# Kernel optimization log

Measured on AMD Instinct MI355X. Metric: run time of the kernel, lower is better.

The kernel has to match this reference:

```python
import jax, jax.numpy as jnp
import numpy as np

N_NODES = 100000
N_EDGES = 1600000
IN_DIM = 128
HID_DIM = 32
OUT_DIM = 64
N_REL = 8
N_CLASSES = 2


def setup_inputs() -> dict:
    key = jax.random.key(0)
    ks = jax.random.split(key, 12)
    x = jax.random.normal(ks[0], (N_NODES, IN_DIM), dtype=jnp.float32)
    edge_index = jax.random.randint(ks[1], (2, N_EDGES), 0, N_NODES, dtype=jnp.int64)
    edge_type = jax.random.randint(ks[2], (N_EDGES,), 0, N_REL, dtype=jnp.int64)
    # FastRGCNConv params: per-relation weight W [R, in, out], root weight, bias
    def glorot(k, shape):
        fan_in, fan_out = shape[-2], shape[-1]
        s = jnp.sqrt(6.0 / (fan_in + fan_out))
        return jax.random.uniform(k, shape, jnp.float32, -s, s)
    W1 = glorot(ks[3], (N_REL, IN_DIM, HID_DIM))
    root1 = glorot(ks[4], (IN_DIM, HID_DIM))
    b1 = jnp.zeros((HID_DIM,), jnp.float32)
    W2 = glorot(ks[5], (N_REL, HID_DIM, OUT_DIM))
    root2 = glorot(ks[6], (HID_DIM, OUT_DIM))
    b2 = jnp.zeros((OUT_DIM,), jnp.float32)
    lin_w = glorot(ks[7], (OUT_DIM, N_CLASSES))
    lin_b = jnp.zeros((N_CLASSES,), jnp.float32)
    return {"x": x, "edge_index": edge_index, "edge_type": edge_type,
            "W1": W1, "root1": root1, "b1": b1,
            "W2": W2, "root2": root2, "b2": b2,
            "lin_w": lin_w, "lin_b": lin_b}


def _fast_rgcn_conv(x, W, root, b, src, dst, etype, n_nodes):
    """FastRGCNConv: per-relation transform, gather by (src, relation),
    mean-aggregate by destination, plus root transform and bias."""
    # Transform all nodes by all relation weights: [N, R, H]
    xW = jnp.einsum('nf,rfh->nrh', x, W)
    # Per-edge message: relation-specific transformed source feature [E, H]
    msg = xW[src, etype]
    agg = jax.ops.segment_sum(msg, dst, num_segments=n_nodes)
    deg = jax.ops.segment_sum(jnp.ones((src.shape[0],), x.dtype), dst,
                              num_segments=n_nodes)
    agg = agg / jnp.maximum(deg, 1.0)[:, None]  # mean aggregation
    return agg + x @ root + b


def reference(x, edge_index, edge_type, W1, root1, b1, W2, root2, b2, lin_w, lin_b):
    src, dst = edge_index[0], edge_index[1]
    n = x.shape[0]
    h = jax.nn.relu(_fast_rgcn_conv(x, W1, root1, b1, src, dst, edge_type, n))
    h = _fast_rgcn_conv(h, W2, root2, b2, src, dst, edge_type, n)
    return h @ lin_w + lin_b
```

## Files before the change

kernel.cpp:

```cpp
#include <hip/hip_runtime.h>

#define NN      100000
#define IN_DIM  128
#define HID     32
#define ODIM    64
#define L1C     288
#define L2K     288
#define NWGS    196
#define NCB     784
#define CCAP    40
#define RECCAP  2304
#define G2ST    296
#define PST     40
#define HST     40

using bf16x8 = __attribute__((ext_vector_type(8))) short;
using f32x4  = __attribute__((ext_vector_type(4))) float;

__device__ __forceinline__ float bf2f(short s) {
    unsigned int u = ((unsigned int)(unsigned short)s) << 16;
    float f; __builtin_memcpy(&f, &u, 4); return f;
}
__device__ __forceinline__ short f2bf(float f) {
    unsigned int u; __builtin_memcpy(&u, &f, 4);
    u += 0x7fffu + ((u >> 16) & 1u);
    return (short)(u >> 16);
}
__device__ __forceinline__ float ldf(const void* p, int i, int f32) {
    return f32 ? ((const float*)p)[i] : bf2f(((const short*)p)[i]);
}
__device__ __forceinline__ int ldi(const int* p, long long i, int i64) {
    return i64 ? p[2 * i] : p[(int)i];
}

__global__ __launch_bounds__(1024) void detect(const short* __restrict__ x,
                                               const short* __restrict__ W1,
                                               const short* __restrict__ r1,
                                               const short* __restrict__ W2,
                                               const short* __restrict__ r2,
                                               const short* __restrict__ lw,
                                               const int* __restrict__ ei,
                                               const int* __restrict__ et,
                                               int* __restrict__ flags) {
    __shared__ int cnt[8];
    if (threadIdx.x < 8) cnt[threadIdx.x] = 0;
    __syncthreads();
    const short* ptrs[6] = {x, W1, r1, W2, r2, lw};
    const int    nsmp[6] = {1024, 1024, 1024, 1024, 1024, 64};
    int t = threadIdx.x;
#pragma unroll
    for (int j = 0; j < 6; ++j) {
        if (t < nsmp[j]) {
            unsigned int s = (unsigned short)ptrs[j][2 * t];
            unsigned int e = (s >> 7) & 0xFF;
            if (e >= 140u || (e >= 1u && e <= 100u)) atomicAdd(&cnt[j], 1);
        }
    }
    if (t < 128) {
        if (ei[2 * t + 1] != 0) atomicAdd(&cnt[6], 1);
        if (et[2 * t + 1] != 0) atomicAdd(&cnt[7], 1);
    }
    __syncthreads();
    if (t == 0) {
        const int ns[6] = {1024, 1024, 1024, 1024, 1024, 64};
        for (int j = 0; j < 6; ++j) flags[j] = (cnt[j] * 4 > ns[j]) ? 1 : 0;
        flags[6] = (cnt[6] == 0) ? 1 : 0;
        flags[7] = (cnt[7] == 0) ? 1 : 0;
    }
}

__global__ __launch_bounds__(256) void prep_w1(const void* __restrict__ W1,
                                               const void* __restrict__ root1,
                                               short* __restrict__ w1t,
                                               const int* __restrict__ flags) {
    int i = blockIdx.x * 256 + threadIdx.x;
    if (i >= L1C * IN_DIM) return;
    int c = i >> 7, f = i & 127;
    float v;
    if (c < 256) { int r = c >> 5, h = c & 31; v = ldf(W1, (r * IN_DIM + f) * HID + h, flags[1]); }
    else         { v = ldf(root1, f * HID + (c - 256), flags[2]); }
    w1t[c * IN_DIM + f] = f2bf(v);
}
__global__ __launch_bounds__(256) void prep_w2c(const void* __restrict__ W2,
                                                const void* __restrict__ root2,
                                                short* __restrict__ w2ct,
                                                const int* __restrict__ flags) {
    int i = blockIdx.x * 256 + threadIdx.x;
    if (i >= ODIM * L2K) return;
    int c = i / L2K, k = i % L2K;
    float v;
    if (k < 256) { int r = k >> 5, kk = k & 31; v = ldf(W2, (r * HID + kk) * ODIM + c, flags[3]); }
    else         { v = ldf(root2, (k - 256) * ODIM + c, flags[4]); }
    w2ct[c * L2K + k] = f2bf(v);
}
__global__ __launch_bounds__(256) void prep_small(const short* __restrict__ b1,
                                                  const short* __restrict__ b2,
                                                  const void* __restrict__ lin_w,
                                                  const short* __restrict__ lin_b,
                                                  short* __restrict__ smallc,
                                                  const int* __restrict__ flags) {
    int i = threadIdx.x;
    if (i < 32)        smallc[i] = b1[i];
    else if (i < 96)   smallc[i] = b2[i - 32];
    else if (i < 224)  smallc[i] = f2bf(ldf(lin_w, i - 96, flags[5]));
    else if (i < 226)  smallc[i] = lin_b[i - 224];
}

__global__ __launch_bounds__(1024) void scatter_coarse(const int* __restrict__ ei,
                                                       const int* __restrict__ et,
                                                       int* __restrict__ cnt,
                                                       int* __restrict__ seg, int E,
                                                       const int* __restrict__ flags) {
    __shared__ int cur[NCB];
    if (threadIdx.x < NCB) cur[threadIdx.x] = 0;
    __syncthreads();
    int i64 = flags[6], t64 = flags[7];
    int epw = (E + NWGS - 1) / NWGS;
    int lo = blockIdx.x * epw;
    int hi = lo + epw; if (hi > E) hi = E;
    for (int i = lo + threadIdx.x; i < hi; i += 1024) {
        int s = ldi(ei, i, i64);
        int d = ldi(ei, (long long)E + i, i64);
        int r = ldi(et, i, t64);
        int cb = d >> 7;
        int pos = atomicAdd(&cur[cb], 1);
        if (pos < CCAP)
            seg[(cb * NWGS + (int)blockIdx.x) * CCAP + pos] = ((d & 127) << 20) | (s << 3) | r;
    }
    __syncthreads();
    if (threadIdx.x < NCB) {
        int c = cur[threadIdx.x];
        cnt[blockIdx.x * NCB + threadIdx.x] = c < CCAP ? c : CCAP;
    }
}

__global__ __launch_bounds__(64) void cb_sum(const int* __restrict__ cnt,
                                             int* __restrict__ cbTot) {
    int cb = blockIdx.x, lane = threadIdx.x;
    int t = 0;
    for (int g = lane; g < NWGS; g += 64) t += cnt[g * NCB + cb];
#pragma unroll
    for (int o = 32; o > 0; o >>= 1) t += __shfl_down(t, o, 64);
    if (lane == 0) cbTot[cb] = t;
}

__global__ __launch_bounds__(1024) void cb_scan2(const int* __restrict__ cbTot,
                                                 int* __restrict__ cbBase,
                                                 int* __restrict__ off) {
    __shared__ int s[1024];
    int t = threadIdx.x;
    int v = (t < NCB) ? cbTot[t] : 0;
    s[t] = v; __syncthreads();
    for (int o = 1; o < 1024; o <<= 1) {
        int u = (t >= o) ? s[t - o] : 0;
        __syncthreads();
        s[t] += u;
        __syncthreads();
    }
    if (t < NCB) cbBase[t] = s[t] - v;
    if (t == NCB - 1) off[NN] = s[t];
}

__global__ __launch_bounds__(256) void build_cb(const int* __restrict__ cnt,
                                                const int* __restrict__ seg,
                                                const int* __restrict__ cbBase,
                                                int* __restrict__ off,
                                                float* __restrict__ inv_deg,
                                                int* __restrict__ packed) {
    __shared__ int cntl[NWGS], soff[NWGS];
    __shared__ int recs[RECCAP];
    __shared__ int degl[128], basel[128], kcur[128];
    __shared__ int stmp[256];
    int cb = blockIdx.x, tid = threadIdx.x;
    if (tid < NWGS) cntl[tid] = cnt[tid * NCB + cb];
    if (tid < 128) degl[tid] = 0;
    __syncthreads();
    int v = (tid < NWGS) ? cntl[tid] : 0;
    stmp[tid] = v; __syncthreads();
    for (int o = 1; o < 256; o <<= 1) {
        int u = (tid >= o) ? stmp[tid - o] : 0;
        __syncthreads();
        stmp[tid] += u;
        __syncthreads();
    }
    if (tid < NWGS) soff[tid] = stmp[tid] - v;
    int tot = stmp[255]; if (tot > RECCAP) tot = RECCAP;
    __syncthreads();
    int wave = tid >> 6, lane = tid & 63;
    for (int g = wave; g < NWGS; g += 4) {
        int c = cntl[g], b = soff[g];
        const int* sp = seg + (cb * NWGS + g) * CCAP;
        for (int e = lane; e < c; e += 64)
            if (b + e < RECCAP) recs[b + e] = sp[e];
    }
    __syncthreads();
    for (int i = tid; i < tot; i += 256) atomicAdd(&degl[recs[i] >> 20], 1);
    __syncthreads();
    int dv = (tid < 128) ? degl[tid] : 0;
    stmp[tid] = dv; __syncthreads();
    for (int o = 1; o < 128; o <<= 1) {
        int u = (tid >= o) ? stmp[tid - o] : 0;
        __syncthreads();
        stmp[tid] += u;
        __syncthreads();
    }
    int gbase = cbBase[cb];
    if (tid < 128) {
        int excl = stmp[tid] - dv;
        basel[tid] = excl;
        kcur[tid] = 0;
        int node = cb * 128 + tid;
        if (node < NN) {
            off[node] = gbase + excl;
            inv_deg[node] = 1.0f / (float)(dv > 1 ? dv : 1);
        }
    }
    __syncthreads();
    for (int i = tid; i < tot; i += 256) {
        int rec = recs[i];
        int n = rec >> 20;
        int p = atomicAdd(&kcur[n], 1);
        packed[gbase + basel[n] + p] = ((n & 15) << 24) | (rec & 0xFFFFF);
    }
}

__global__ __launch_bounds__(256) void gemm1(const void* __restrict__ x,
                                             const short* __restrict__ w1t,
                                             short* __restrict__ xw,
                                             const int* __restrict__ flags) {
    int wave = threadIdx.x >> 6, lane = threadIdx.x & 63;
    int m = lane & 15, quad = lane >> 4;
    int row0 = (blockIdx.x * 4 + wave) * 64;
    if (row0 >= NN) return;

    bf16x8 a[4][4];
    int fp32 = flags[0];
#pragma unroll
    for (int t = 0; t < 4; ++t) {
        int row = row0 + t * 16 + m;
        int rc = row < NN ? row : NN - 1;
        if (fp32) {
            const float* xr = (const float*)x + rc * IN_DIM + quad * 8;
#pragma unroll
            for (int kt = 0; kt < 4; ++kt) {
                const f32x4* q = (const f32x4*)(xr + kt * 32);
                f32x4 u0 = q[0], u1 = q[1];
                bf16x8 tt;
                tt[0] = f2bf(u0[0]); tt[1] = f2bf(u0[1]); tt[2] = f2bf(u0[2]); tt[3] = f2bf(u0[3]);
                tt[4] = f2bf(u1[0]); tt[5] = f2bf(u1[1]); tt[6] = f2bf(u1[2]); tt[7] = f2bf(u1[3]);
                a[t][kt] = tt;
            }
        } else {
            const short* xr = (const short*)x + rc * IN_DIM + quad * 8;
#pragma unroll
            for (int kt = 0; kt < 4; ++kt) a[t][kt] = *(const bf16x8*)(xr + kt * 32);
        }
    }

    for (int ct = 0; ct < 18; ++ct) {
        const short* wp = w1t + (ct * 16 + m) * IN_DIM + quad * 8;
        bf16x8 b[4];
#pragma unroll
        for (int kt = 0; kt < 4; ++kt) b[kt] = *(const bf16x8*)(wp + kt * 32);
#pragma unroll
        for (int t = 0; t < 4; ++t) {
            f32x4 acc = {0.f, 0.f, 0.f, 0.f};
#pragma unroll
            for (int kt = 0; kt < 4; ++kt)
                acc = __builtin_amdgcn_mfma_f32_16x16x32_bf16(a[t][kt], b[kt], acc, 0, 0, 0);
#pragma unroll
            for (int i = 0; i < 4; ++i) {
                int r = row0 + t * 16 + quad * 4 + i;
                if (r < NN) xw[r * L1C + ct * 16 + m] = f2bf(acc[i]);
            }
        }
    }
}

__global__ __launch_bounds__(256) void agg1(const short* __restrict__ xw,
                                            const int* __restrict__ off,
                                            const int* __restrict__ packed,
                                            const float* __restrict__ inv_deg,
                                            const short* __restrict__ smallc,
                                            short* __restrict__ h) {
    int lane = threadIdx.x & 31;
    int node = blockIdx.x * 8 + (threadIdx.x >> 5);
    if (node >= NN) return;
    int s = off[node], e = off[node + 1];
    float acc = 0.f;
    int i = s;
    for (; i + 3 < e; i += 4) {
        int pk0 = packed[i], pk1 = packed[i + 1], pk2 = packed[i + 2], pk3 = packed[i + 3];
        float v0 = bf2f(xw[((pk0 >> 3) & 0x1FFFF) * L1C + (pk0 & 7) * 32 + lane]);
        float v1 = bf2f(xw[((pk1 >> 3) & 0x1FFFF) * L1C + (pk1 & 7) * 32 + lane]);
        float v2 = bf2f(xw[((pk2 >> 3) & 0x1FFFF) * L1C + (pk2 & 7) * 32 + lane]);
        float v3 = bf2f(xw[((pk3 >> 3) & 0x1FFFF) * L1C + (pk3 & 7) * 32 + lane]);
        acc += (v0 + v1) + (v2 + v3);
    }
    for (; i < e; ++i) {
        int pk = packed[i];
        acc += bf2f(xw[((pk >> 3) & 0x1FFFF) * L1C + (pk & 7) * 32 + lane]);
    }
    float v = acc * inv_deg[node] + bf2f(xw[node * L1C + 256 + lane]) + bf2f(smallc[lane]);
    h[node * HID + lane] = f2bf(v > 0.f ? v : 0.f);
}

__global__ __launch_bounds__(256) void agg2_fused(const short* __restrict__ h,
                                                  const int* __restrict__ off,
                                                  const int* __restrict__ packed,
                                                  const float* __restrict__ inv_deg,
                                                  const short* __restrict__ w2ct,
                                                  const short* __restrict__ smallc,
                                                  float* __restrict__ out) {
    __shared__ __align__(16) short Pl[128 * PST];
    __shared__ __align__(16) short HgT[32 * HST];
    __shared__ __align__(16) short g2l[16 * G2ST];
    __shared__ float red[4][16][2];
    __shared__ float invl[16];
    int tid = threadIdx.x;
    int row0 = blockIdx.x * 16;
    if (tid < 16) invl[tid] = inv_deg[row0 + tid];
    int st = off[row0], en = off[row0 + 16];

    int wave = tid >> 6, lane = tid & 63;
    int m15 = lane & 15, quad = lane >> 4;
    int e = tid & 31;
    int part = tid >> 5;

    {
        uint4 z = {0, 0, 0, 0};
        uint4* pz = (uint4*)Pl;
#pragma unroll
        for (int j = 0; j < 2; ++j) pz[tid + j * 256] = z;
        if (tid < 128) pz[tid + 512] = z;
    }

    f32x4 acc00 = {0,0,0,0}, acc01 = {0,0,0,0}, acc10 = {0,0,0,0}, acc11 = {0,0,0,0};
    int prevrow = -1;

    for (int c0 = st; c0 < en; c0 += 32) {
        int idx = c0 + e;
        int pk = (idx < en) ? packed[idx] : 0;
        int src = (pk >> 3) & 0x1FFFF;
        uint2 hv = *(const uint2*)(h + src * HID + part * 4);
        __syncthreads();
        if (tid < 32 && prevrow >= 0) Pl[prevrow * PST + e] = 0;
        short hs0 = (short)(hv.x & 0xFFFF), hs1 = (short)(hv.x >> 16);
        short hs2 = (short)(hv.y & 0xFFFF), hs3 = (short)(hv.y >> 16);
        HgT[(part * 4 + 0) * HST + e] = hs0;
        HgT[(part * 4 + 1) * HST + e] = hs1;
        HgT[(part * 4 + 2) * HST + e] = hs2;
        HgT[(part * 4 + 3) * HST + e] = hs3;
        if (tid < 32) {
            if (idx < en) {
                int row = ((pk >> 24) & 15) * 8 + (pk & 7);
                Pl[row * PST + e] = (short)0x3F80;
                prevrow = row;
            } else prevrow = -1;
        }
        __syncthreads();
        bf16x8 a0 = *(const bf16x8*)(&HgT[m15 * HST + quad * 8]);
        bf16x8 a1 = *(const bf16x8*)(&HgT[(m15 + 16) * HST + quad * 8]);
        bf16x8 b0 = *(const bf16x8*)(&Pl[((wave * 2 + 0) * 16 + m15) * PST + quad * 8]);
        bf16x8 b1 = *(const bf16x8*)(&Pl[((wave * 2 + 1) * 16 + m15) * PST + quad * 8]);
        acc00 = __builtin_amdgcn_mfma_f32_16x16x32_bf16(a0, b0, acc00, 0, 0, 0);
        acc10 = __builtin_amdgcn_mfma_f32_16x16x32_bf16(a1, b0, acc10, 0, 0, 0);
        acc01 = __builtin_amdgcn_mfma_f32_16x16x32_bf16(a0, b1, acc01, 0, 0, 0);
        acc11 = __builtin_amdgcn_mfma_f32_16x16x32_bf16(a1, b1, acc11, 0, 0, 0);
    }
    __syncthreads();

    {
        int nr0 = (wave * 2 + 0) * 16 + m15;
        int nr1 = (wave * 2 + 1) * 16 + m15;
        float sc0 = invl[nr0 >> 3], sc1 = invl[nr1 >> 3];
        int d0 = quad * 4;
#pragma unroll
        for (int i = 0; i < 4; ++i) {
            g2l[(nr0 >> 3) * G2ST + (nr0 & 7) * 32 + d0 + i]      = f2bf(acc00[i] * sc0);
            g2l[(nr0 >> 3) * G2ST + (nr0 & 7) * 32 + 16 + d0 + i] = f2bf(acc10[i] * sc0);
            g2l[(nr1 >> 3) * G2ST + (nr1 & 7) * 32 + d0 + i]      = f2bf(acc01[i] * sc1);
            g2l[(nr1 >> 3) * G2ST + (nr1 & 7) * 32 + 16 + d0 + i] = f2bf(acc11[i] * sc1);
        }
    }
    for (int j = tid; j < 16 * 32; j += 256) {
        int node = j >> 5, d = j & 31;
        g2l[node * G2ST + 256 + d] = h[(row0 + node) * HID + d];
    }
    __syncthreads();

    const short* wp = w2ct + (wave * 16 + m15) * L2K + quad * 8;
    bf16x8 a[9], b[9];
#pragma unroll
    for (int kt = 0; kt < 9; ++kt) {
        b[kt] = *(const bf16x8*)(wp + kt * 32);
        a[kt] = *(const bf16x8*)(&g2l[m15 * G2ST + quad * 8 + kt * 32]);
    }
    f32x4 acc = {0.f, 0.f, 0.f, 0.f};
#pragma unroll
    for (int kt = 0; kt < 9; ++kt)
        acc = __builtin_amdgcn_mfma_f32_16x16x32_bf16(a[kt], b[kt], acc, 0, 0, 0);

    int c = wave * 16 + m15;
    float lw0 = bf2f(smallc[96 + c * 2 + 0]);
    float lw1 = bf2f(smallc[96 + c * 2 + 1]);
    float b2c = bf2f(smallc[32 + c]);
    float pr0[4], pr1[4];
#pragma unroll
    for (int i = 0; i < 4; ++i) {
        float v = acc[i] + b2c;
        pr0[i] = v * lw0;
        pr1[i] = v * lw1;
    }
#pragma unroll
    for (int o = 1; o < 16; o <<= 1) {
#pragma unroll
        for (int i = 0; i < 4; ++i) {
            pr0[i] += __shfl_xor(pr0[i], o, 64);
            pr1[i] += __shfl_xor(pr1[i], o, 64);
        }
    }
    if (m15 == 0) {
#pragma unroll
        for (int i = 0; i < 4; ++i) {
            red[wave][quad * 4 + i][0] = pr0[i];
            red[wave][quad * 4 + i][1] = pr1[i];
        }
    }
    __syncthreads();
    if (tid < 32) {
        int row = tid >> 1, j = tid & 1;
        float v = red[0][row][j] + red[1][row][j] + red[2][row][j] + red[3][row][j]
                + bf2f(smallc[224 + j]);
        out[(row0 + row) * 2 + j] = v;
    }
}

extern "C" void kernel_launch(void* const* d_in, const int* in_sizes, int n_in,
                              void* d_out, int out_size, void* d_ws, size_t ws_size,
                              hipStream_t stream) {
    const void* x     = d_in[0];
    const int*  ei    = (const int*)d_in[1];
    const int*  etype = (const int*)d_in[2];
    const void* W1    = d_in[3];
    const void* root1 = d_in[4];
    const void* b1    = d_in[5];
    const void* W2    = d_in[6];
    const void* root2 = d_in[7];
    const void* b2    = d_in[8];
    const void* lin_w = d_in[9];
    const void* lin_b = d_in[10];
    float* out = (float*)d_out;

    const int E = in_sizes[2];

    char* p = (char*)d_ws;
    auto alloc = [&](size_t bytes) { char* r = p; p += (bytes + 255) & ~(size_t)255; return (void*)r; };
    int*   flags   = (int*)  alloc(256);
    int*   off     = (int*)  alloc((size_t)(NN + 1) * 4);
    float* inv_deg = (float*)alloc((size_t)NN * 4);
    int*   packed  = (int*)  alloc((size_t)E * 4);
    int*   cnt     = (int*)  alloc((size_t)NWGS * NCB * 4);
    int*   cbTot   = (int*)  alloc((size_t)NCB * 4);
    int*   cbBase  = (int*)  alloc((size_t)NCB * 4);
    int*   seg     = (int*)  alloc((size_t)NCB * NWGS * CCAP * 4);
    short* w1t     = (short*)alloc((size_t)L1C * IN_DIM * 2);
    short* w2ct    = (short*)alloc((size_t)ODIM * L2K * 2);
    short* smallc  = (short*)alloc(256 * 2);
    short* h       = (short*)alloc((size_t)NN * HID * 2);
    short* xw1     = (short*)alloc((size_t)NN * L1C * 2);

    detect<<<1, 1024, 0, stream>>>((const short*)x, (const short*)W1, (const short*)root1,
                                   (const short*)W2, (const short*)root2, (const short*)lin_w,
                                   ei, etype, flags);
    prep_w1<<<(L1C * IN_DIM + 255) / 256, 256, 0, stream>>>(W1, root1, w1t, flags);
    prep_w2c<<<(ODIM * L2K + 255) / 256, 256, 0, stream>>>(W2, root2, w2ct, flags);
    prep_small<<<1, 256, 0, stream>>>((const short*)b1, (const short*)b2, lin_w,
                                      (const short*)lin_b, smallc, flags);

    scatter_coarse<<<NWGS, 1024, 0, stream>>>(ei, etype, cnt, seg, E, flags);
    cb_sum<<<NCB, 64, 0, stream>>>(cnt, cbTot);
    cb_scan2<<<1, 1024, 0, stream>>>(cbTot, cbBase, off);
    build_cb<<<NCB, 256, 0, stream>>>(cnt, seg, cbBase, off, inv_deg, packed);

    gemm1<<<((NN + 63) / 64 + 3) / 4, 256, 0, stream>>>(x, w1t, xw1, flags);
    agg1<<<(NN + 7) / 8, 256, 0, stream>>>(xw1, off, packed, inv_deg, smallc, h);
    agg2_fused<<<NN / 16, 256, 0, stream>>>(h, off, packed, inv_deg, w2ct, smallc, out);
}
```

Measured before the change: 310.1 us.

## Merge weight-prep kernels and co-launch gemm1 with edge scatter; unroll agg1 by 8

Folds the three weight-preparation kernels into one launch. It also moves the independent edge coarse-scatter into the same grid as the first GEMM, using extra blocks, so the two overlap on the GPU and fewer kernels are launched. The scatter blocks drop from 1024 to 256 threads, so each scatter block processes its edge slice more slowly. agg1 gains an 8-way unrolled gather loop to keep more loads in flight.

```diff
diff --git a/kernel.cpp b/kernel.cpp
--- a/kernel.cpp
+++ b/kernel.cpp
@@ -69,68 +69,124 @@
     }
 }
 
-__global__ __launch_bounds__(256) void prep_w1(const void* __restrict__ W1,
-                                               const void* __restrict__ root1,
-                                               short* __restrict__ w1t,
-                                               const int* __restrict__ flags) {
-    int i = blockIdx.x * 256 + threadIdx.x;
-    if (i >= L1C * IN_DIM) return;
-    int c = i >> 7, f = i & 127;
-    float v;
-    if (c < 256) { int r = c >> 5, h = c & 31; v = ldf(W1, (r * IN_DIM + f) * HID + h, flags[1]); }
-    else         { v = ldf(root1, f * HID + (c - 256), flags[2]); }
-    w1t[c * IN_DIM + f] = f2bf(v);
-}
-__global__ __launch_bounds__(256) void prep_w2c(const void* __restrict__ W2,
+__global__ __launch_bounds__(256) void prep_all(const void* __restrict__ W1,
+                                                const void* __restrict__ root1,
+                                                const void* __restrict__ W2,
                                                 const void* __restrict__ root2,
+                                                const short* __restrict__ b1,
+                                                const short* __restrict__ b2,
+                                                const void* __restrict__ lin_w,
+                                                const short* __restrict__ lin_b,
+                                                short* __restrict__ w1t,
                                                 short* __restrict__ w2ct,
+                                                short* __restrict__ smallc,
                                                 const int* __restrict__ flags) {
-    int i = blockIdx.x * 256 + threadIdx.x;
-    if (i >= ODIM * L2K) return;
-    int c = i / L2K, k = i % L2K;
-    float v;
-    if (k < 256) { int r = k >> 5, kk = k & 31; v = ldf(W2, (r * HID + kk) * ODIM + c, flags[3]); }
-    else         { v = ldf(root2, (k - 256) * ODIM + c, flags[4]); }
-    w2ct[c * L2K + k] = f2bf(v);
-}
-__global__ __launch_bounds__(256) void prep_small(const short* __restrict__ b1,
-                                                  const short* __restrict__ b2,
-                                                  const void* __restrict__ lin_w,
-                                                  const short* __restrict__ lin_b,
-                                                  short* __restrict__ smallc,
-                                                  const int* __restrict__ flags) {
-    int i = threadIdx.x;
-    if (i < 32)        smallc[i] = b1[i];
-    else if (i < 96)   smallc[i] = b2[i - 32];
-    else if (i < 224)  smallc[i] = f2bf(ldf(lin_w, i - 96, flags[5]));
-    else if (i < 226)  smallc[i] = lin_b[i - 224];
-}
-
-__global__ __launch_bounds__(1024) void scatter_coarse(const int* __restrict__ ei,
-                                                       const int* __restrict__ et,
-                                                       int* __restrict__ cnt,
-                                                       int* __restrict__ seg, int E,
-                                                       const int* __restrict__ flags) {
-    __shared__ int cur[NCB];
-    if (threadIdx.x < NCB) cur[threadIdx.x] = 0;
-    __syncthreads();
-    int i64 = flags[6], t64 = flags[7];
-    int epw = (E + NWGS - 1) / NWGS;
-    int lo = blockIdx.x * epw;
-    int hi = lo + epw; if (hi > E) hi = E;
-    for (int i = lo + threadIdx.x; i < hi; i += 1024) {
-        int s = ldi(ei, i, i64);
-        int d = ldi(ei, (long long)E + i, i64);
-        int r = ldi(et, i, t64);
-        int cb = d >> 7;
-        int pos = atomicAdd(&cur[cb], 1);
-        if (pos < CCAP)
-            seg[(cb * NWGS + (int)blockIdx.x) * CCAP + pos] = ((d & 127) << 20) | (s << 3) | r;
-    }
-    __syncthreads();
-    if (threadIdx.x < NCB) {
-        int c = cur[threadIdx.x];
-        cnt[blockIdx.x * NCB + threadIdx.x] = c < CCAP ? c : CCAP;
+    int gi = blockIdx.x * 256 + threadIdx.x;
+    if (gi < L1C * IN_DIM) {
+        int c = gi >> 7, f = gi & 127;
+        float v;
+        if (c < 256) { int r = c >> 5, h = c & 31; v = ldf(W1, (r * IN_DIM + f) * HID + h, flags[1]); }
+        else         { v = ldf(root1, f * HID + (c - 256), flags[2]); }
+        w1t[c * IN_DIM + f] = f2bf(v);
+        return;
+    }
+    int i2 = gi - L1C * IN_DIM;
+    if (i2 < ODIM * L2K) {
+        int c = i2 / L2K, k = i2 % L2K;
+        float v;
+        if (k < 256) { int r = k >> 5, kk = k & 31; v = ldf(W2, (r * HID + kk) * ODIM + c, flags[3]); }
+        else         { v = ldf(root2, (k - 256) * ODIM + c, flags[4]); }
+        w2ct[c * L2K + k] = f2bf(v);
+        return;
+    }
+    int i3 = i2 - ODIM * L2K;
+    if (i3 < 256) {
+        if (i3 < 32)        smallc[i3] = b1[i3];
+        else if (i3 < 96)   smallc[i3] = b2[i3 - 32];
+        else if (i3 < 224)  smallc[i3] = f2bf(ldf(lin_w, i3 - 96, flags[5]));
+        else if (i3 < 226)  smallc[i3] = lin_b[i3 - 224];
+    }
+}
+
+__global__ __launch_bounds__(256) void gemm1_scatter(const void* __restrict__ x,
+                                                     const short* __restrict__ w1t,
+                                                     short* __restrict__ xw,
+                                                     const int* __restrict__ ei,
+                                                     const int* __restrict__ et,
+                                                     int* __restrict__ cnt,
+                                                     int* __restrict__ seg, int E,
+                                                     const int* __restrict__ flags, int G1) {
+    if ((int)blockIdx.x >= G1) {
+        __shared__ int cur[NCB];
+        for (int k = threadIdx.x; k < NCB; k += 256) cur[k] = 0;
+        __syncthreads();
+        int bid = blockIdx.x - G1;
+        int i64 = flags[6], t64 = flags[7];
+        int epw = (E + NWGS - 1) / NWGS;
+        int lo = bid * epw;
+        int hi = lo + epw; if (hi > E) hi = E;
+        for (int i = lo + threadIdx.x; i < hi; i += 256) {
+            int s = ldi(ei, i, i64);
+            int d = ldi(ei, (long long)E + i, i64);
+            int r = ldi(et, i, t64);
+            int cb = d >> 7;
+            int pos = atomicAdd(&cur[cb], 1);
+            if (pos < CCAP)
+                seg[(cb * NWGS + bid) * CCAP + pos] = ((d & 127) << 20) | (s << 3) | r;
+        }
+        __syncthreads();
+        for (int k = threadIdx.x; k < NCB; k += 256) {
+            int c = cur[k];
+            cnt[bid * NCB + k] = c < CCAP ? c : CCAP;
+        }
+        return;
+    }
+    int wave = threadIdx.x >> 6, lane = threadIdx.x & 63;
+    int m = lane & 15, quad = lane >> 4;
+    int row0 = (blockIdx.x * 4 + wave) * 64;
+    if (row0 >= NN) return;
+
+    bf16x8 a[4][4];
+    int fp32 = flags[0];
+#pragma unroll
+    for (int t = 0; t < 4; ++t) {
+        int row = row0 + t * 16 + m;
+        int rc = row < NN ? row : NN - 1;
+        if (fp32) {
+            const float* xr = (const float*)x + rc * IN_DIM + quad * 8;
+#pragma unroll
+            for (int kt = 0; kt < 4; ++kt) {
+                const f32x4* q = (const f32x4*)(xr + kt * 32);
+                f32x4 u0 = q[0], u1 = q[1];
+                bf16x8 tt;
+                tt[0] = f2bf(u0[0]); tt[1] = f2bf(u0[1]); tt[2] = f2bf(u0[2]); tt[3] = f2bf(u0[3]);
+                tt[4] = f2bf(u1[0]); tt[5] = f2bf(u1[1]); tt[6] = f2bf(u1[2]); tt[7] = f2bf(u1[3]);
+                a[t][kt] = tt;
+            }
+        } else {
+            const short* xr = (const short*)x + rc * IN_DIM + quad * 8;
+#pragma unroll
+            for (int kt = 0; kt < 4; ++kt) a[t][kt] = *(const bf16x8*)(xr + kt * 32);
+        }
+    }
+
+    for (int ct = 0; ct < 18; ++ct) {
+        const short* wp = w1t + (ct * 16 + m) * IN_DIM + quad * 8;
+        bf16x8 b[4];
+#pragma unroll
+        for (int kt = 0; kt < 4; ++kt) b[kt] = *(const bf16x8*)(wp + kt * 32);
+#pragma unroll
+        for (int t = 0; t < 4; ++t) {
+            f32x4 acc = {0.f, 0.f, 0.f, 0.f};
+#pragma unroll
+            for (int kt = 0; kt < 4; ++kt)
+                acc = __builtin_amdgcn_mfma_f32_16x16x32_bf16(a[t][kt], b[kt], acc, 0, 0, 0);
+#pragma unroll
+            for (int i = 0; i < 4; ++i) {
+                int r = row0 + t * 16 + quad * 4 + i;
+                if (r < NN) xw[r * L1C + ct * 16 + m] = f2bf(acc[i]);
+            }
+        }
     }
 }
 
@@ -224,59 +280,6 @@
     }
 }
 
-__global__ __launch_bounds__(256) void gemm1(const void* __restrict__ x,
-                                             const short* __restrict__ w1t,
-                                             short* __restrict__ xw,
-                                             const int* __restrict__ flags) {
-    int wave = threadIdx.x >> 6, lane = threadIdx.x & 63;
-    int m = lane & 15, quad = lane >> 4;
-    int row0 = (blockIdx.x * 4 + wave) * 64;
-    if (row0 >= NN) return;
-
-    bf16x8 a[4][4];
-    int fp32 = flags[0];
-#pragma unroll
-    for (int t = 0; t < 4; ++t) {
-        int row = row0 + t * 16 + m;
-        int rc = row < NN ? row : NN - 1;
-        if (fp32) {
-            const float* xr = (const float*)x + rc * IN_DIM + quad * 8;
-#pragma unroll
-            for (int kt = 0; kt < 4; ++kt) {
-                const f32x4* q = (const f32x4*)(xr + kt * 32);
-                f32x4 u0 = q[0], u1 = q[1];
-                bf16x8 tt;
-                tt[0] = f2bf(u0[0]); tt[1] = f2bf(u0[1]); tt[2] = f2bf(u0[2]); tt[3] = f2bf(u0[3]);
-                tt[4] = f2bf(u1[0]); tt[5] = f2bf(u1[1]); tt[6] = f2bf(u1[2]); tt[7] = f2bf(u1[3]);
-                a[t][kt] = tt;
-            }
-        } else {
-            const short* xr = (const short*)x + rc * IN_DIM + quad * 8;
-#pragma unroll
-            for (int kt = 0; kt < 4; ++kt) a[t][kt] = *(const bf16x8*)(xr + kt * 32);
-        }
-    }
-
-    for (int ct = 0; ct < 18; ++ct) {
-        const short* wp = w1t + (ct * 16 + m) * IN_DIM + quad * 8;
-        bf16x8 b[4];
-#pragma unroll
-        for (int kt = 0; kt < 4; ++kt) b[kt] = *(const bf16x8*)(wp + kt * 32);
-#pragma unroll
-        for (int t = 0; t < 4; ++t) {
-            f32x4 acc = {0.f, 0.f, 0.f, 0.f};
-#pragma unroll
-            for (int kt = 0; kt < 4; ++kt)
-                acc = __builtin_amdgcn_mfma_f32_16x16x32_bf16(a[t][kt], b[kt], acc, 0, 0, 0);
-#pragma unroll
-            for (int i = 0; i < 4; ++i) {
-                int r = row0 + t * 16 + quad * 4 + i;
-                if (r < NN) xw[r * L1C + ct * 16 + m] = f2bf(acc[i]);
-            }
-        }
-    }
-}
-
 __global__ __launch_bounds__(256) void agg1(const short* __restrict__ xw,
                                             const int* __restrict__ off,
                                             const int* __restrict__ packed,
@@ -289,6 +292,19 @@
     int s = off[node], e = off[node + 1];
     float acc = 0.f;
     int i = s;
+    for (; i + 7 < e; i += 8) {
+        int pk0 = packed[i],     pk1 = packed[i + 1], pk2 = packed[i + 2], pk3 = packed[i + 3];
+        int pk4 = packed[i + 4], pk5 = packed[i + 5], pk6 = packed[i + 6], pk7 = packed[i + 7];
+        float v0 = bf2f(xw[((pk0 >> 3) & 0x1FFFF) * L1C + (pk0 & 7) * 32 + lane]);
+        float v1 = bf2f(xw[((pk1 >> 3) & 0x1FFFF) * L1C + (pk1 & 7) * 32 + lane]);
+        float v2 = bf2f(xw[((pk2 >> 3) & 0x1FFFF) * L1C + (pk2 & 7) * 32 + lane]);
+        float v3 = bf2f(xw[((pk3 >> 3) & 0x1FFFF) * L1C + (pk3 & 7) * 32 + lane]);
+        float v4 = bf2f(xw[((pk4 >> 3) & 0x1FFFF) * L1C + (pk4 & 7) * 32 + lane]);
+        float v5 = bf2f(xw[((pk5 >> 3) & 0x1FFFF) * L1C + (pk5 & 7) * 32 + lane]);
+        float v6 = bf2f(xw[((pk6 >> 3) & 0x1FFFF) * L1C + (pk6 & 7) * 32 + lane]);
+        float v7 = bf2f(xw[((pk7 >> 3) & 0x1FFFF) * L1C + (pk7 & 7) * 32 + lane]);
+        acc += ((v0 + v1) + (v2 + v3)) + ((v4 + v5) + (v6 + v7));
+    }
     for (; i + 3 < e; i += 4) {
         int pk0 = packed[i], pk1 = packed[i + 1], pk2 = packed[i + 2], pk3 = packed[i + 3];
         float v0 = bf2f(xw[((pk0 >> 3) & 0x1FFFF) * L1C + (pk0 & 7) * 32 + lane]);
@@ -473,17 +489,19 @@
     detect<<<1, 1024, 0, stream>>>((const short*)x, (const short*)W1, (const short*)root1,
                                    (const short*)W2, (const short*)root2, (const short*)lin_w,
                                    ei, etype, flags);
-    prep_w1<<<(L1C * IN_DIM + 255) / 256, 256, 0, stream>>>(W1, root1, w1t, flags);
-    prep_w2c<<<(ODIM * L2K + 255) / 256, 256, 0, stream>>>(W2, root2, w2ct, flags);
-    prep_small<<<1, 256, 0, stream>>>((const short*)b1, (const short*)b2, lin_w,
-                                      (const short*)lin_b, smallc, flags);
-
-    scatter_coarse<<<NWGS, 1024, 0, stream>>>(ei, etype, cnt, seg, E, flags);
+    const int prep_items = L1C * IN_DIM + ODIM * L2K + 256;
+    prep_all<<<(prep_items + 255) / 256, 256, 0, stream>>>(W1, root1, W2, root2,
+                                                           (const short*)b1, (const short*)b2,
+                                                           lin_w, (const short*)lin_b,
+                                                           w1t, w2ct, smallc, flags);
+
+    const int G1 = ((NN + 63) / 64 + 3) / 4;
+    gemm1_scatter<<<G1 + NWGS, 256, 0, stream>>>(x, w1t, xw1, ei, etype,
+                                                 cnt, seg, E, flags, G1);
     cb_sum<<<NCB, 64, 0, stream>>>(cnt, cbTot);
     cb_scan2<<<1, 1024, 0, stream>>>(cbTot, cbBase, off);
     build_cb<<<NCB, 256, 0, stream>>>(cnt, seg, cbBase, off, inv_deg, packed);
 
-    gemm1<<<((NN + 63) / 64 + 3) / 4, 256, 0, stream>>>(x, w1t, xw1, flags);
     agg1<<<(NN + 7) / 8, 256, 0, stream>>>(xw1, off, packed, inv_deg, smallc, h);
     agg2_fused<<<NN / 16, 256, 0, stream>>>(h, off, packed, inv_deg, w2ct, smallc, out);
 }
```

Result: slower. 335.3 us (+8.1%).
